# Optimization experiments

Measured on AMD Instinct MI355X. Metric: run time of the kernel, lower is better.

Reference implementation:

```python
import jax, jax.numpy as jnp
import numpy as np

B, N, DIM = 2, 2048, 1024
HEADS, DIM_HEAD, ROT = 16, 64, 32
SCALE = DIM_HEAD ** -0.5
INNER = HEADS * DIM_HEAD


def rotate_half(x):
    # '... (j d) -> ... j d' with j=2 -> split into first/second half
    d = x.shape[-1] // 2
    x1, x2 = x[..., :d], x[..., d:]
    return jnp.concatenate([-x2, x1], axis=-1)


def apply_rotary_pos_emb(freqs, t):
    rot = freqs.shape[-1]
    t1, t_pass = t[..., :rot], t[..., rot:]
    t1 = t1 * jnp.cos(freqs) + rotate_half(t1) * jnp.sin(freqs)
    return jnp.concatenate([t1, t_pass], axis=-1)


def setup_inputs() -> dict:
    key = jax.random.key(0)
    ks = jax.random.split(key, 5)
    x = jax.random.normal(ks[0], (B, N, DIM), dtype=jnp.float32)
    mask = jnp.ones((B, N), dtype=bool)
    rotary_pos_emb = jax.random.normal(ks[1], (N, ROT), dtype=jnp.float32)
    w_qkv = jax.random.normal(ks[2], (DIM, 3 * INNER), dtype=jnp.float32) * (DIM ** -0.5)
    w_out = jax.random.normal(ks[3], (INNER, DIM), dtype=jnp.float32) * (INNER ** -0.5)
    g = jnp.ones((DIM,), dtype=jnp.float32)
    return {"x": x, "mask": mask, "rotary_pos_emb": rotary_pos_emb,
            "w_qkv": w_qkv, "w_out": w_out, "g": g}


def reference(x, mask, rotary_pos_emb, w_qkv, w_out, g):
    b, n, _ = x.shape
    qkv = x @ w_qkv  # [b, n, 3*inner]
    q, k, v = jnp.split(qkv, 3, axis=-1)
    def to_heads(t):
        return t.reshape(b, n, HEADS, DIM_HEAD).transpose(0, 2, 1, 3)  # b h n d
    q, k, v = to_heads(q), to_heads(k), to_heads(v)
    q = q * SCALE
    # note: original applies rotary to q, k AND v
    q = apply_rotary_pos_emb(rotary_pos_emb, q)
    k = apply_rotary_pos_emb(rotary_pos_emb, k)
    v = apply_rotary_pos_emb(rotary_pos_emb, v)
    sim = jnp.einsum('bhid,bhjd->bhij', q, k)  # [b, h, n, n]
    neg = -jnp.finfo(sim.dtype).max
    sim = jnp.where(mask[:, None, None, :], sim, neg)
    causal_mask = jnp.triu(jnp.ones((n, n), dtype=bool), 1)
    sim = jnp.where(causal_mask, neg, sim)
    attn = jax.nn.softmax(sim.astype(jnp.float32), axis=-1).astype(sim.dtype)
    out = jnp.einsum('bhij,bhjd->bhid', attn, v)
    out = out.transpose(0, 2, 1, 3).reshape(b, n, INNER)
    out = out @ w_out
    # LayerNorm (no bias), eps=1e-5 for fp32, biased variance
    mean = jnp.mean(out, axis=-1, keepdims=True)
    var = jnp.var(out, axis=-1, keepdims=True)
    return (out - mean) * jax.lax.rsqrt(var + 1e-5) * g
```

## Files before the change

kernel.cpp:

```cpp
#include <hip/hip_runtime.h>
#include <stdint.h>

typedef unsigned short u16;
typedef __bf16 bf16x8 __attribute__((ext_vector_type(8)));
typedef float f32x4 __attribute__((ext_vector_type(4)));

#define B_ 2
#define N_ 2048
#define H_ 16
#define SCALE_ 0.125f
#define FM_ 11.0f

__device__ __forceinline__ float b2f(u16 u) {
    unsigned v = (unsigned)u << 16;
    float f;
    __builtin_memcpy(&f, &v, 4);
    return f;
}
__device__ __forceinline__ u16 f2b(float f) {
    unsigned x;
    __builtin_memcpy(&x, &f, 4);
    x = x + 0x7fff + ((x >> 16) & 1);
    return (u16)(x >> 16);
}
__device__ __forceinline__ unsigned fbits(float f) {
    unsigned x;
    __builtin_memcpy(&x, &f, 4);
    return x;
}

typedef const __attribute__((address_space(1))) unsigned int ga_uint;
typedef __attribute__((address_space(3))) unsigned int ls_uint;
__device__ __forceinline__ void gld_lds16(const void* g, void* l) {
    __builtin_amdgcn_global_load_lds((ga_uint*)g, (ls_uint*)l, 16, 0, 0);
}

#define MFMA_ __builtin_amdgcn_mfma_f32_16x16x32_bf16
#define ZERO4_ ((f32x4){0.f, 0.f, 0.f, 0.f})

__global__ __launch_bounds__(256) void sentinel(float* __restrict__ out, int n, float val) {
    int i = blockIdx.x * 256 + threadIdx.x;
    if (i < n) out[i] = val;
}

__global__ __launch_bounds__(256) void prep(const float* __restrict__ rotf,
                                            float* __restrict__ ct, float* __restrict__ st,
                                            const float* __restrict__ x, u16* __restrict__ xbf,
                                            const float* __restrict__ wqkv, u16* __restrict__ wqkvT,
                                            const float* __restrict__ wout, u16* __restrict__ woutT) {
    __shared__ float tile[32][33];
    int bid = blockIdx.x;
    const int tid = threadIdx.x;
    if (bid < 256) {
        int i = bid * 256 + tid;
        float f = rotf[i];
        ct[i] = cosf(f);
        st[i] = sinf(f);
        return;
    }
    bid -= 256;
    if (bid < 4096) {
        int i = (bid * 256 + tid) * 4;
        float4 v = *(const float4*)(x + i);
        ushort4 o;
        o.x = f2b(v.x); o.y = f2b(v.y); o.z = f2b(v.z); o.w = f2b(v.w);
        *(ushort4*)(xbf + i) = o;
        return;
    }
    bid -= 4096;
    const float* in;
    u16* out;
    int C, bx, by;
    if (bid < 3072) {
        in = wqkv; out = wqkvT; C = 3072; bx = bid % 96; by = bid / 96;
    } else {
        bid -= 3072;
        in = wout; out = woutT; C = 1024; bx = bid % 32; by = bid / 32;
    }
    const int R = 1024;
    int tx = tid & 31, ty = tid >> 5;
    int c0 = bx * 32, r0 = by * 32;
#pragma unroll
    for (int i = 0; i < 32; i += 8) tile[ty + i][tx] = in[(size_t)(r0 + ty + i) * C + c0 + tx];
    __syncthreads();
#pragma unroll
    for (int i = 0; i < 32; i += 8) out[(size_t)(c0 + ty + i) * R + r0 + tx] = f2b(tile[tx][ty + i]);
}

__global__ __launch_bounds__(256) void gemm_qkv(const u16* __restrict__ A, const u16* __restrict__ Bt,
                                                const float* __restrict__ ct, const float* __restrict__ st,
                                                u16* __restrict__ qo, u16* __restrict__ ko,
                                                u16* __restrict__ vt) {
    __shared__ __align__(16) u16 As[2][128 * 32];
    __shared__ __align__(16) u16 Bs[2][128 * 32];
    const int tid = threadIdx.x;
    const int wave = tid >> 6, lane = tid & 63;
    const int l15 = lane & 15, q4 = lane >> 4;
    const int id = blockIdx.x;
    const int xcd = id & 7, slot = id >> 3;
    const int nt = (xcd & 1) * 12 + (slot % 12);
    const int mt = (xcd >> 1) * 8 + (slot / 12);
    const int m0 = mt * 128, n0 = nt * 128;
    const int wm = (wave & 1) * 64, wn = (wave >> 1) * 64;
    const int lrow = lane >> 2, lchunk = (lane & 3) * 8;

    auto stage = [&](int buf, int k0) {
        int r0_ = wave * 32, r1_ = r0_ + 16;
        gld_lds16(&A[(size_t)(m0 + r0_ + lrow) * 1024 + k0 + lchunk], &As[buf][r0_ * 32]);
        gld_lds16(&Bt[(size_t)(n0 + r0_ + lrow) * 1024 + k0 + lchunk], &Bs[buf][r0_ * 32]);
        gld_lds16(&A[(size_t)(m0 + r1_ + lrow) * 1024 + k0 + lchunk], &As[buf][r1_ * 32]);
        gld_lds16(&Bt[(size_t)(n0 + r1_ + lrow) * 1024 + k0 + lchunk], &Bs[buf][r1_ * 32]);
    };

    f32x4 c00 = ZERO4_, c01 = ZERO4_, c02 = ZERO4_, c03 = ZERO4_;
    f32x4 c10 = ZERO4_, c11 = ZERO4_, c12 = ZERO4_, c13 = ZERO4_;
    f32x4 c20 = ZERO4_, c21 = ZERO4_, c22 = ZERO4_, c23 = ZERO4_;
    f32x4 c30 = ZERO4_, c31 = ZERO4_, c32 = ZERO4_, c33 = ZERO4_;

    stage(0, 0);
    __syncthreads();
    for (int t = 0; t < 32; ++t) {
        const int cur = t & 1;
        if (t < 31) stage(cur ^ 1, (t + 1) * 32);
        bf16x8 a0 = *(const bf16x8*)&As[cur][(wm + l15) * 32 + q4 * 8];
        bf16x8 a1 = *(const bf16x8*)&As[cur][(wm + 16 + l15) * 32 + q4 * 8];
        bf16x8 a2 = *(const bf16x8*)&As[cur][(wm + 32 + l15) * 32 + q4 * 8];
        bf16x8 a3 = *(const bf16x8*)&As[cur][(wm + 48 + l15) * 32 + q4 * 8];
        bf16x8 b0 = *(const bf16x8*)&Bs[cur][(wn + l15) * 32 + q4 * 8];
        bf16x8 b1 = *(const bf16x8*)&Bs[cur][(wn + 16 + l15) * 32 + q4 * 8];
        bf16x8 b2 = *(const bf16x8*)&Bs[cur][(wn + 32 + l15) * 32 + q4 * 8];
        bf16x8 b3 = *(const bf16x8*)&Bs[cur][(wn + 48 + l15) * 32 + q4 * 8];
        c00 = MFMA_(a0, b0, c00, 0, 0, 0); c01 = MFMA_(a0, b1, c01, 0, 0, 0);
        c02 = MFMA_(a0, b2, c02, 0, 0, 0); c03 = MFMA_(a0, b3, c03, 0, 0, 0);
        c10 = MFMA_(a1, b0, c10, 0, 0, 0); c11 = MFMA_(a1, b1, c11, 0, 0, 0);
        c12 = MFMA_(a1, b2, c12, 0, 0, 0); c13 = MFMA_(a1, b3, c13, 0, 0, 0);
        c20 = MFMA_(a2, b0, c20, 0, 0, 0); c21 = MFMA_(a2, b1, c21, 0, 0, 0);
        c22 = MFMA_(a2, b2, c22, 0, 0, 0); c23 = MFMA_(a2, b3, c23, 0, 0, 0);
        c30 = MFMA_(a3, b0, c30, 0, 0, 0); c31 = MFMA_(a3, b1, c31, 0, 0, 0);
        c32 = MFMA_(a3, b2, c32, 0, 0, 0); c33 = MFMA_(a3, b3, c33, 0, 0, 0);
        if (t < 31) __syncthreads();
    }
    const int qh = n0 + wn;
    const int t = qh >> 10;
    const int h = (qh & 1023) >> 6;
    auto epi = [&](int mtb, f32x4 x0v, f32x4 x1v, f32x4 x2v, f32x4 x3v) {
#pragma unroll
        for (int r = 0; r < 4; r++) {
            int gm = m0 + wm + mtb + q4 * 4 + r;
            int b = gm >> 11, n = gm & 2047;
            float x0 = x0v[r], x1 = x1v[r], x2 = x2v[r], x3 = x3v[r];
            float c1 = ct[n * 32 + l15], s1 = st[n * 32 + l15];
            float c2 = ct[n * 32 + 16 + l15], s2 = st[n * 32 + 16 + l15];
            if (t == 0) { x0 *= SCALE_; x1 *= SCALE_; x2 *= SCALE_; x3 *= SCALE_; }
            float r0 = x0 * c1 - x1 * s1;
            float r1 = x1 * c2 + x0 * s2;
            int bh = b * H_ + h;
            if (t == 2) {
                u16* o = vt + (size_t)bh * 64 * N_;
                o[(l15) * N_ + n] = f2b(r0);
                o[(l15 + 16) * N_ + n] = f2b(r1);
                o[(l15 + 32) * N_ + n] = f2b(x2);
                o[(l15 + 48) * N_ + n] = f2b(x3);
            } else {
                u16* dst = (t == 0) ? qo : ko;
                u16* p = dst + ((size_t)bh * N_ + n) * 64;
                p[l15] = f2b(r0);
                p[l15 + 16] = f2b(r1);
                p[l15 + 32] = f2b(x2);
                p[l15 + 48] = f2b(x3);
            }
        }
    };
    epi(0, c00, c01, c02, c03);
    epi(16, c10, c11, c12, c13);
    epi(32, c20, c21, c22, c23);
    epi(48, c30, c31, c32, c33);
}

__global__ __launch_bounds__(256) void attn(const u16* __restrict__ q, const u16* __restrict__ k,
                                            const u16* __restrict__ vt, u16* __restrict__ out) {
    __shared__ __align__(16) u16 Ks[2][64 * 72];
    __shared__ __align__(16) u16 Vs[2][64 * 72];
    __shared__ __align__(16) u16 Ps[64 * 72];
    const int tid = threadIdx.x, wave = tid >> 6, lane = tid & 63;
    const int l15 = lane & 15, q4 = lane >> 4;
    const int id = blockIdx.x;
    const int slot = id >> 3;
    const int bh = (id & 7) * 4 + (slot >> 4);
    const int ta = slot & 15, tb = 31 - ta;
    const u16* qp = q + (size_t)bh * N_ * 64;
    const u16* kp = k + (size_t)bh * N_ * 64;
    const u16* vp = vt + (size_t)bh * 64 * N_;
    const int b = bh >> 4, h = bh & 15;
    const int srow8 = tid >> 3, scol8 = (tid & 7) * 8;
    const int prow = (wave * 16 + l15) * 72;

    bf16x8 aqA0, aqA1, aqB0, aqB1;
    {
        int qr = ta * 64 + wave * 16;
        aqA0 = *(const bf16x8*)&qp[(qr + l15) * 64 + q4 * 8];
        aqA1 = *(const bf16x8*)&qp[(qr + l15) * 64 + 32 + q4 * 8];
        qr = tb * 64 + wave * 16;
        aqB0 = *(const bf16x8*)&qp[(qr + l15) * 64 + q4 * 8];
        aqB1 = *(const bf16x8*)&qp[(qr + l15) * 64 + 32 + q4 * 8];
    }
    f32x4 o[4];
#pragma unroll
    for (int i = 0; i < 4; i++) o[i] = ZERO4_;
    float psum = 0.f;

    uint4 LK0, LK1, LV0, LV1;
    auto ldissue = [&](int jt) {
        LK0 = *(const uint4*)&kp[(size_t)(jt * 64 + srow8) * 64 + scol8];
        LK1 = *(const uint4*)&kp[(size_t)(jt * 64 + 32 + srow8) * 64 + scol8];
        LV0 = *(const uint4*)&vp[(size_t)srow8 * N_ + jt * 64 + scol8];
        LV1 = *(const uint4*)&vp[(size_t)(32 + srow8) * N_ + jt * 64 + scol8];
    };
    auto wrbuf = [&](int buf) {
        *(uint4*)&Ks[buf][srow8 * 72 + scol8] = LK0;
        *(uint4*)&Ks[buf][(32 + srow8) * 72 + scol8] = LK1;
        *(uint4*)&Vs[buf][srow8 * 72 + scol8] = LV0;
        *(uint4*)&Vs[buf][(32 + srow8) * 72 + scol8] = LV1;
    };
    auto tileof = [&](int i) { return (i <= ta) ? i : i - ta - 1; };

    auto iter = [&](bf16x8 aq0, bf16x8 aq1, int cur, int domask, int qa, int jb) {
#pragma unroll
        for (int kt = 0; kt < 4; kt++) {
            bf16x8 kf0 = *(const bf16x8*)&Ks[cur][(kt * 16 + l15) * 72 + q4 * 8];
            bf16x8 kf1 = *(const bf16x8*)&Ks[cur][(kt * 16 + l15) * 72 + 32 + q4 * 8];
            f32x4 z = ZERO4_;
            z = MFMA_(kf0, aq0, z, 0, 0, 0);
            z = MFMA_(kf1, aq1, z, 0, 0, 0);
            float p0, p1, p2, p3;
            {
                float s0 = z[0], s1 = z[1], s2 = z[2], s3 = z[3];
                if (domask) {
                    int key = jb * 64 + kt * 16 + q4 * 4;
                    if (key + 0 > qa) s0 = -1e30f;
                    if (key + 1 > qa) s1 = -1e30f;
                    if (key + 2 > qa) s2 = -1e30f;
                    if (key + 3 > qa) s3 = -1e30f;
                }
                p0 = __expf(s0 - FM_); p1 = __expf(s1 - FM_);
                p2 = __expf(s2 - FM_); p3 = __expf(s3 - FM_);
            }
            psum += (p0 + p1) + (p2 + p3);
            uint2 pk;
            pk.x = __builtin_amdgcn_perm(fbits(p1), fbits(p0), 0x07060302u);
            pk.y = __builtin_amdgcn_perm(fbits(p3), fbits(p2), 0x07060302u);
            *(uint2*)&Ps[prow + kt * 16 + q4 * 4] = pk;
        }
        bf16x8 pf0 = *(const bf16x8*)&Ps[prow + q4 * 8];
        bf16x8 pf1 = *(const bf16x8*)&Ps[prow + 32 + q4 * 8];
#pragma unroll
        for (int dt = 0; dt < 4; dt++) {
            bf16x8 v0 = *(const bf16x8*)&Vs[cur][(dt * 16 + l15) * 72 + q4 * 8];
            bf16x8 v1 = *(const bf16x8*)&Vs[cur][(dt * 16 + l15) * 72 + 32 + q4 * 8];
            o[dt] = MFMA_(v0, pf0, o[dt], 0, 0, 0);
            o[dt] = MFMA_(v1, pf1, o[dt], 0, 0, 0);
        }
    };
    auto epilogue = [&](int qt) {
        float v = psum;
        v += __shfl_xor(v, 16);
        v += __shfl_xor(v, 32);
        float inv = 1.f / v;
        int n = qt * 64 + wave * 16 + l15;
        u16* op = out + ((size_t)b * N_ + n) * 1024 + h * 64;
#pragma unroll
        for (int dt = 0; dt < 4; dt++) {
            union { u16 u[4]; uint2 v2; } w;
#pragma unroll
            for (int r = 0; r < 4; r++) w.u[r] = f2b(o[dt][r] * inv);
            *(uint2*)(op + dt * 16 + q4 * 4) = w.v2;
        }
#pragma unroll
        for (int i = 0; i < 4; i++) o[i] = ZERO4_;
        psum = 0.f;
    };

    ldissue(0);
    wrbuf(0);
    ldissue(tileof(1));
    int m = 0;
    for (int jb = 0; jb <= ta; jb++, m++) {
        const int cur = m & 1;
        asm volatile("s_waitcnt lgkmcnt(0)" ::: "memory");
        __builtin_amdgcn_s_barrier();
        iter(aqA0, aqA1, cur, jb == ta, ta * 64 + wave * 16 + l15, jb);
        wrbuf(cur ^ 1);
        ldissue(tileof(m + 2));
    }
    epilogue(ta);
    for (int jb = 0; jb <= tb; jb++, m++) {
        const int cur = m & 1;
        asm volatile("s_waitcnt lgkmcnt(0)" ::: "memory");
        __builtin_amdgcn_s_barrier();
        iter(aqB0, aqB1, cur, jb == tb, tb * 64 + wave * 16 + l15, jb);
        if (m < 32) {
            wrbuf(cur ^ 1);
            if (m < 31) ldissue(tileof(m + 2));
        }
    }
    epilogue(tb);
}

__global__ __launch_bounds__(256) void gemm_out(const u16* __restrict__ A, const u16* __restrict__ Bt,
                                                float* __restrict__ C) {
    __shared__ __align__(16) u16 As[2][128 * 32];
    __shared__ __align__(16) u16 Bs[2][128 * 32];
    const int tid = threadIdx.x;
    const int wave = tid >> 6, lane = tid & 63;
    const int l15 = lane & 15, q4 = lane >> 4;
    const int id = blockIdx.x;
    const int xcd = id & 7, slot = id >> 3;
    const int mt = xcd * 4 + (slot >> 3);
    const int nt = slot & 7;
    const int m0 = mt * 128, n0 = nt * 128;
    const int wm = (wave & 1) * 64, wn = (wave >> 1) * 64;
    const int lrow = lane >> 2, lchunk = (lane & 3) * 8;

    auto stage = [&](int buf, int k0) {
        int r0_ = wave * 32, r1_ = r0_ + 16;
        gld_lds16(&A[(size_t)(m0 + r0_ + lrow) * 1024 + k0 + lchunk], &As[buf][r0_ * 32]);
        gld_lds16(&Bt[(size_t)(n0 + r0_ + lrow) * 1024 + k0 + lchunk], &Bs[buf][r0_ * 32]);
        gld_lds16(&A[(size_t)(m0 + r1_ + lrow) * 1024 + k0 + lchunk], &As[buf][r1_ * 32]);
        gld_lds16(&Bt[(size_t)(n0 + r1_ + lrow) * 1024 + k0 + lchunk], &Bs[buf][r1_ * 32]);
    };

    f32x4 c00 = ZERO4_, c01 = ZERO4_, c02 = ZERO4_, c03 = ZERO4_;
    f32x4 c10 = ZERO4_, c11 = ZERO4_, c12 = ZERO4_, c13 = ZERO4_;
    f32x4 c20 = ZERO4_, c21 = ZERO4_, c22 = ZERO4_, c23 = ZERO4_;
    f32x4 c30 = ZERO4_, c31 = ZERO4_, c32 = ZERO4_, c33 = ZERO4_;

    stage(0, 0);
    __syncthreads();
    for (int t = 0; t < 32; ++t) {
        const int cur = t & 1;
        if (t < 31) stage(cur ^ 1, (t + 1) * 32);
        bf16x8 a0 = *(const bf16x8*)&As[cur][(wm + l15) * 32 + q4 * 8];
        bf16x8 a1 = *(const bf16x8*)&As[cur][(wm + 16 + l15) * 32 + q4 * 8];
        bf16x8 a2 = *(const bf16x8*)&As[cur][(wm + 32 + l15) * 32 + q4 * 8];
        bf16x8 a3 = *(const bf16x8*)&As[cur][(wm + 48 + l15) * 32 + q4 * 8];
        bf16x8 b0 = *(const bf16x8*)&Bs[cur][(wn + l15) * 32 + q4 * 8];
        bf16x8 b1 = *(const bf16x8*)&Bs[cur][(wn + 16 + l15) * 32 + q4 * 8];
        bf16x8 b2 = *(const bf16x8*)&Bs[cur][(wn + 32 + l15) * 32 + q4 * 8];
        bf16x8 b3 = *(const bf16x8*)&Bs[cur][(wn + 48 + l15) * 32 + q4 * 8];
        c00 = MFMA_(a0, b0, c00, 0, 0, 0); c01 = MFMA_(a0, b1, c01, 0, 0, 0);
        c02 = MFMA_(a0, b2, c02, 0, 0, 0); c03 = MFMA_(a0, b3, c03, 0, 0, 0);
        c10 = MFMA_(a1, b0, c10, 0, 0, 0); c11 = MFMA_(a1, b1, c11, 0, 0, 0);
        c12 = MFMA_(a1, b2, c12, 0, 0, 0); c13 = MFMA_(a1, b3, c13, 0, 0, 0);
        c20 = MFMA_(a2, b0, c20, 0, 0, 0); c21 = MFMA_(a2, b1, c21, 0, 0, 0);
        c22 = MFMA_(a2, b2, c22, 0, 0, 0); c23 = MFMA_(a2, b3, c23, 0, 0, 0);
        c30 = MFMA_(a3, b0, c30, 0, 0, 0); c31 = MFMA_(a3, b1, c31, 0, 0, 0);
        c32 = MFMA_(a3, b2, c32, 0, 0, 0); c33 = MFMA_(a3, b3, c33, 0, 0, 0);
        if (t < 31) __syncthreads();
    }
    auto sto = [&](int mtb, int ntb, f32x4 c) {
#pragma unroll
        for (int r = 0; r < 4; r++) {
            int gm = m0 + wm + mtb + q4 * 4 + r;
            int gn = n0 + wn + ntb + l15;
            C[(size_t)gm * 1024 + gn] = c[r];
        }
    };
    sto(0, 0, c00);  sto(0, 16, c01);  sto(0, 32, c02);  sto(0, 48, c03);
    sto(16, 0, c10); sto(16, 16, c11); sto(16, 32, c12); sto(16, 48, c13);
    sto(32, 0, c20); sto(32, 16, c21); sto(32, 32, c22); sto(32, 48, c23);
    sto(48, 0, c30); sto(48, 16, c31); sto(48, 32, c32); sto(48, 48, c33);
}

__global__ __launch_bounds__(256) void lnorm(const float* __restrict__ x, const float* __restrict__ g,
                                             float* __restrict__ out) {
    __shared__ float sh[8];
    int row = blockIdx.x, tid = threadIdx.x;
    float4 v = *(const float4*)(x + (size_t)row * 1024 + tid * 4);
    float s = v.x + v.y + v.z + v.w;
    float sq = v.x * v.x + v.y * v.y + v.z * v.z + v.w * v.w;
#pragma unroll
    for (int m = 1; m < 64; m <<= 1) {
        s += __shfl_xor(s, m);
        sq += __shfl_xor(sq, m);
    }
    if ((tid & 63) == 0) {
        sh[tid >> 6] = s;
        sh[4 + (tid >> 6)] = sq;
    }
    __syncthreads();
    s = sh[0] + sh[1] + sh[2] + sh[3];
    sq = sh[4] + sh[5] + sh[6] + sh[7];
    float mean = s * (1.f / 1024.f);
    float var = fmaxf(sq * (1.f / 1024.f) - mean * mean, 0.f);
    float rstd = rsqrtf(var + 1e-5f);
    float4 gv = *(const float4*)(g + tid * 4);
    float4 ov;
    ov.x = (v.x - mean) * rstd * gv.x;
    ov.y = (v.y - mean) * rstd * gv.y;
    ov.z = (v.z - mean) * rstd * gv.z;
    ov.w = (v.w - mean) * rstd * gv.w;
    *(float4*)(out + (size_t)row * 1024 + tid * 4) = ov;
}

extern "C" void kernel_launch(void* const* d_in, const int* in_sizes, int n_in,
                              void* d_out, int out_size, void* d_ws, size_t ws_size,
                              hipStream_t stream) {
    const float* x = nullptr;
    const float* rotf = nullptr;
    const float* wqkv = nullptr;
    const float* wout = nullptr;
    const float* g = nullptr;
    for (int i = 0; i < n_in; i++) {
        switch (in_sizes[i]) {
            case 4194304: x = (const float*)d_in[i]; break;
            case 65536:   rotf = (const float*)d_in[i]; break;
            case 3145728: wqkv = (const float*)d_in[i]; break;
            case 1048576: wout = (const float*)d_in[i]; break;
            case 1024:    g = (const float*)d_in[i]; break;
            default: break;
        }
    }
    int oblk = (out_size + 255) / 256;
    if (!(x && rotf && wqkv && wout && g)) {
        sentinel<<<oblk, 256, 0, stream>>>((float*)d_out, out_size, 200.f);
        return;
    }
    const size_t MB = 1024u * 1024;
    if (ws_size < 80 * MB) {
        sentinel<<<oblk, 256, 0, stream>>>((float*)d_out, out_size, 100.f);
        return;
    }
    char* ws = (char*)d_ws;
    u16* wqkvT = (u16*)(ws);
    u16* woutT = (u16*)(ws + 6 * MB);
    u16* xbf = (u16*)(ws + 8 * MB);
    u16* qbuf = (u16*)(ws + 16 * MB);
    u16* kbuf = (u16*)(ws + 24 * MB);
    u16* vtbuf = (u16*)(ws + 32 * MB);
    u16* abuf = (u16*)(ws + 40 * MB);
    float* pbuf = (float*)(ws + 48 * MB);
    float* ctab = (float*)(ws + 64 * MB);
    float* stab = (float*)(ws + 64 * MB + 256 * 1024);

    prep<<<8448, 256, 0, stream>>>(rotf, ctab, stab, x, xbf, wqkv, wqkvT, wout, woutT);
    gemm_qkv<<<768, 256, 0, stream>>>(xbf, wqkvT, ctab, stab, qbuf, kbuf, vtbuf);
    attn<<<512, 256, 0, stream>>>(qbuf, kbuf, vtbuf, abuf);
    gemm_out<<<256, 256, 0, stream>>>(abuf, woutT, pbuf);
    lnorm<<<4096, 256, 0, stream>>>(pbuf, g, (float*)d_out);
}
```

Measured before the change: 201.3 us.

## Swizzle GEMM LDS tiles and drop double buffering in qkv/out GEMMs

Both projection GEMMs now write global-to-LDS loads into an XOR-swizzled layout. The loading lanes' global addresses are remapped by an inverse swizzle, and the MFMA operand reads use swizzled offsets, to avoid LDS bank conflicts on the 16-byte fragment reads. The double-buffered prefetch is replaced by a single buffer with load, sync, compute, sync each K step. This halves LDS use and may raise occupancy, but global-load latency is no longer overlapped with MFMA work within a block.

```diff
diff --git a/kernel.cpp b/kernel.cpp
--- a/kernel.cpp
+++ b/kernel.cpp
@@ -87,12 +87,21 @@
     for (int i = 0; i < 32; i += 8) out[(size_t)(c0 + ty + i) * R + r0 + tx] = f2b(tile[tx][ty + i]);
 }
 
+__device__ __forceinline__ int swz_off(int row, int c16) {
+    return (((row * 64 + c16 * 16) ^ ((row & 7) << 4)) >> 1);
+}
+__device__ __forceinline__ void swz_inv(int W, int& r, int& c16) {
+    int rh = W >> 7;
+    r = (rh << 1) | (((W >> 6) & 1) ^ ((rh >> 1) & 1));
+    c16 = ((W >> 4) & 3) ^ (r & 3);
+}
+
 __global__ __launch_bounds__(256) void gemm_qkv(const u16* __restrict__ A, const u16* __restrict__ Bt,
                                                 const float* __restrict__ ct, const float* __restrict__ st,
                                                 u16* __restrict__ qo, u16* __restrict__ ko,
                                                 u16* __restrict__ vt) {
-    __shared__ __align__(16) u16 As[2][128 * 32];
-    __shared__ __align__(16) u16 Bs[2][128 * 32];
+    __shared__ __align__(16) u16 As[128 * 32];
+    __shared__ __align__(16) u16 Bs[128 * 32];
     const int tid = threadIdx.x;
     const int wave = tid >> 6, lane = tid & 63;
     const int l15 = lane & 15, q4 = lane >> 4;
@@ -102,34 +111,39 @@
     const int mt = (xcd >> 1) * 8 + (slot / 12);
     const int m0 = mt * 128, n0 = nt * 128;
     const int wm = (wave & 1) * 64, wn = (wave >> 1) * 64;
-    const int lrow = lane >> 2, lchunk = (lane & 3) * 8;
-
-    auto stage = [&](int buf, int k0) {
-        int r0_ = wave * 32, r1_ = r0_ + 16;
-        gld_lds16(&A[(size_t)(m0 + r0_ + lrow) * 1024 + k0 + lchunk], &As[buf][r0_ * 32]);
-        gld_lds16(&Bt[(size_t)(n0 + r0_ + lrow) * 1024 + k0 + lchunk], &Bs[buf][r0_ * 32]);
-        gld_lds16(&A[(size_t)(m0 + r1_ + lrow) * 1024 + k0 + lchunk], &As[buf][r1_ * 32]);
-        gld_lds16(&Bt[(size_t)(n0 + r1_ + lrow) * 1024 + k0 + lchunk], &Bs[buf][r1_ * 32]);
-    };
+
+    int rS0, cS0, rS1, cS1;
+    swz_inv((wave * 32) * 64 + lane * 16, rS0, cS0);
+    swz_inv((wave * 32 + 16) * 64 + lane * 16, rS1, cS1);
+    const u16* aS0 = A + (size_t)(m0 + rS0) * 1024 + cS0 * 8;
+    const u16* aS1 = A + (size_t)(m0 + rS1) * 1024 + cS1 * 8;
+    const u16* bS0 = Bt + (size_t)(n0 + rS0) * 1024 + cS0 * 8;
+    const u16* bS1 = Bt + (size_t)(n0 + rS1) * 1024 + cS1 * 8;
+
+    const int oa0 = swz_off(wm + l15, q4), oa1 = swz_off(wm + 16 + l15, q4),
+              oa2 = swz_off(wm + 32 + l15, q4), oa3 = swz_off(wm + 48 + l15, q4);
+    const int ob0 = swz_off(wn + l15, q4), ob1 = swz_off(wn + 16 + l15, q4),
+              ob2 = swz_off(wn + 32 + l15, q4), ob3 = swz_off(wn + 48 + l15, q4);
 
     f32x4 c00 = ZERO4_, c01 = ZERO4_, c02 = ZERO4_, c03 = ZERO4_;
     f32x4 c10 = ZERO4_, c11 = ZERO4_, c12 = ZERO4_, c13 = ZERO4_;
     f32x4 c20 = ZERO4_, c21 = ZERO4_, c22 = ZERO4_, c23 = ZERO4_;
     f32x4 c30 = ZERO4_, c31 = ZERO4_, c32 = ZERO4_, c33 = ZERO4_;
 
-    stage(0, 0);
-    __syncthreads();
-    for (int t = 0; t < 32; ++t) {
-        const int cur = t & 1;
-        if (t < 31) stage(cur ^ 1, (t + 1) * 32);
-        bf16x8 a0 = *(const bf16x8*)&As[cur][(wm + l15) * 32 + q4 * 8];
-        bf16x8 a1 = *(const bf16x8*)&As[cur][(wm + 16 + l15) * 32 + q4 * 8];
-        bf16x8 a2 = *(const bf16x8*)&As[cur][(wm + 32 + l15) * 32 + q4 * 8];
-        bf16x8 a3 = *(const bf16x8*)&As[cur][(wm + 48 + l15) * 32 + q4 * 8];
-        bf16x8 b0 = *(const bf16x8*)&Bs[cur][(wn + l15) * 32 + q4 * 8];
-        bf16x8 b1 = *(const bf16x8*)&Bs[cur][(wn + 16 + l15) * 32 + q4 * 8];
-        bf16x8 b2 = *(const bf16x8*)&Bs[cur][(wn + 32 + l15) * 32 + q4 * 8];
-        bf16x8 b3 = *(const bf16x8*)&Bs[cur][(wn + 48 + l15) * 32 + q4 * 8];
+    for (int k0 = 0; k0 < 1024; k0 += 32) {
+        gld_lds16(aS0 + k0, &As[(wave * 32) * 32]);
+        gld_lds16(bS0 + k0, &Bs[(wave * 32) * 32]);
+        gld_lds16(aS1 + k0, &As[(wave * 32 + 16) * 32]);
+        gld_lds16(bS1 + k0, &Bs[(wave * 32 + 16) * 32]);
+        __syncthreads();
+        bf16x8 a0 = *(const bf16x8*)&As[oa0];
+        bf16x8 a1 = *(const bf16x8*)&As[oa1];
+        bf16x8 a2 = *(const bf16x8*)&As[oa2];
+        bf16x8 a3 = *(const bf16x8*)&As[oa3];
+        bf16x8 b0 = *(const bf16x8*)&Bs[ob0];
+        bf16x8 b1 = *(const bf16x8*)&Bs[ob1];
+        bf16x8 b2 = *(const bf16x8*)&Bs[ob2];
+        bf16x8 b3 = *(const bf16x8*)&Bs[ob3];
         c00 = MFMA_(a0, b0, c00, 0, 0, 0); c01 = MFMA_(a0, b1, c01, 0, 0, 0);
         c02 = MFMA_(a0, b2, c02, 0, 0, 0); c03 = MFMA_(a0, b3, c03, 0, 0, 0);
         c10 = MFMA_(a1, b0, c10, 0, 0, 0); c11 = MFMA_(a1, b1, c11, 0, 0, 0);
@@ -138,7 +152,7 @@
         c22 = MFMA_(a2, b2, c22, 0, 0, 0); c23 = MFMA_(a2, b3, c23, 0, 0, 0);
         c30 = MFMA_(a3, b0, c30, 0, 0, 0); c31 = MFMA_(a3, b1, c31, 0, 0, 0);
         c32 = MFMA_(a3, b2, c32, 0, 0, 0); c33 = MFMA_(a3, b3, c33, 0, 0, 0);
-        if (t < 31) __syncthreads();
+        __syncthreads();
     }
     const int qh = n0 + wn;
     const int t = qh >> 10;
@@ -308,8 +322,8 @@
 
 __global__ __launch_bounds__(256) void gemm_out(const u16* __restrict__ A, const u16* __restrict__ Bt,
                                                 float* __restrict__ C) {
-    __shared__ __align__(16) u16 As[2][128 * 32];
-    __shared__ __align__(16) u16 Bs[2][128 * 32];
+    __shared__ __align__(16) u16 As[128 * 32];
+    __shared__ __align__(16) u16 Bs[128 * 32];
     const int tid = threadIdx.x;
     const int wave = tid >> 6, lane = tid & 63;
     const int l15 = lane & 15, q4 = lane >> 4;
@@ -319,34 +333,39 @@
     const int nt = slot & 7;
     const int m0 = mt * 128, n0 = nt * 128;
     const int wm = (wave & 1) * 64, wn = (wave >> 1) * 64;
-    const int lrow = lane >> 2, lchunk = (lane & 3) * 8;
-
-    auto stage = [&](int buf, int k0) {
-        int r0_ = wave * 32, r1_ = r0_ + 16;
-        gld_lds16(&A[(size_t)(m0 + r0_ + lrow) * 1024 + k0 + lchunk], &As[buf][r0_ * 32]);
-        gld_lds16(&Bt[(size_t)(n0 + r0_ + lrow) * 1024 + k0 + lchunk], &Bs[buf][r0_ * 32]);
-        gld_lds16(&A[(size_t)(m0 + r1_ + lrow) * 1024 + k0 + lchunk], &As[buf][r1_ * 32]);
-        gld_lds16(&Bt[(size_t)(n0 + r1_ + lrow) * 1024 + k0 + lchunk], &Bs[buf][r1_ * 32]);
-    };
+
+    int rS0, cS0, rS1, cS1;
+    swz_inv((wave * 32) * 64 + lane * 16, rS0, cS0);
+    swz_inv((wave * 32 + 16) * 64 + lane * 16, rS1, cS1);
+    const u16* aS0 = A + (size_t)(m0 + rS0) * 1024 + cS0 * 8;
+    const u16* aS1 = A + (size_t)(m0 + rS1) * 1024 + cS1 * 8;
+    const u16* bS0 = Bt + (size_t)(n0 + rS0) * 1024 + cS0 * 8;
+    const u16* bS1 = Bt + (size_t)(n0 + rS1) * 1024 + cS1 * 8;
+
+    const int oa0 = swz_off(wm + l15, q4), oa1 = swz_off(wm + 16 + l15, q4),
+              oa2 = swz_off(wm + 32 + l15, q4), oa3 = swz_off(wm + 48 + l15, q4);
+    const int ob0 = swz_off(wn + l15, q4), ob1 = swz_off(wn + 16 + l15, q4),
+              ob2 = swz_off(wn + 32 + l15, q4), ob3 = swz_off(wn + 48 + l15, q4);
 
     f32x4 c00 = ZERO4_, c01 = ZERO4_, c02 = ZERO4_, c03 = ZERO4_;
     f32x4 c10 = ZERO4_, c11 = ZERO4_, c12 = ZERO4_, c13 = ZERO4_;
     f32x4 c20 = ZERO4_, c21 = ZERO4_, c22 = ZERO4_, c23 = ZERO4_;
     f32x4 c30 = ZERO4_, c31 = ZERO4_, c32 = ZERO4_, c33 = ZERO4_;
 
-    stage(0, 0);
-    __syncthreads();
-    for (int t = 0; t < 32; ++t) {
-        const int cur = t & 1;
-        if (t < 31) stage(cur ^ 1, (t + 1) * 32);
-        bf16x8 a0 = *(const bf16x8*)&As[cur][(wm + l15) * 32 + q4 * 8];
-        bf16x8 a1 = *(const bf16x8*)&As[cur][(wm + 16 + l15) * 32 + q4 * 8];
-        bf16x8 a2 = *(const bf16x8*)&As[cur][(wm + 32 + l15) * 32 + q4 * 8];
-        bf16x8 a3 = *(const bf16x8*)&As[cur][(wm + 48 + l15) * 32 + q4 * 8];
-        bf16x8 b0 = *(const bf16x8*)&Bs[cur][(wn + l15) * 32 + q4 * 8];
-        bf16x8 b1 = *(const bf16x8*)&Bs[cur][(wn + 16 + l15) * 32 + q4 * 8];
-        bf16x8 b2 = *(const bf16x8*)&Bs[cur][(wn + 32 + l15) * 32 + q4 * 8];
-        bf16x8 b3 = *(const bf16x8*)&Bs[cur][(wn + 48 + l15) * 32 + q4 * 8];
+    for (int k0 = 0; k0 < 1024; k0 += 32) {
+        gld_lds16(aS0 + k0, &As[(wave * 32) * 32]);
+        gld_lds16(bS0 + k0, &Bs[(wave * 32) * 32]);
+        gld_lds16(aS1 + k0, &As[(wave * 32 + 16) * 32]);
+        gld_lds16(bS1 + k0, &Bs[(wave * 32 + 16) * 32]);
+        __syncthreads();
+        bf16x8 a0 = *(const bf16x8*)&As[oa0];
+        bf16x8 a1 = *(const bf16x8*)&As[oa1];
+        bf16x8 a2 = *(const bf16x8*)&As[oa2];
+        bf16x8 a3 = *(const bf16x8*)&As[oa3];
+        bf16x8 b0 = *(const bf16x8*)&Bs[ob0];
+        bf16x8 b1 = *(const bf16x8*)&Bs[ob1];
+        bf16x8 b2 = *(const bf16x8*)&Bs[ob2];
+        bf16x8 b3 = *(const bf16x8*)&Bs[ob3];
         c00 = MFMA_(a0, b0, c00, 0, 0, 0); c01 = MFMA_(a0, b1, c01, 0, 0, 0);
         c02 = MFMA_(a0, b2, c02, 0, 0, 0); c03 = MFMA_(a0, b3, c03, 0, 0, 0);
         c10 = MFMA_(a1, b0, c10, 0, 0, 0); c11 = MFMA_(a1, b1, c11, 0, 0, 0);
@@ -355,7 +374,7 @@
         c22 = MFMA_(a2, b2, c22, 0, 0, 0); c23 = MFMA_(a2, b3, c23, 0, 0, 0);
         c30 = MFMA_(a3, b0, c30, 0, 0, 0); c31 = MFMA_(a3, b1, c31, 0, 0, 0);
         c32 = MFMA_(a3, b2, c32, 0, 0, 0); c33 = MFMA_(a3, b3, c33, 0, 0, 0);
-        if (t < 31) __syncthreads();
+        __syncthreads();
     }
     auto sto = [&](int mtb, int ntb, f32x4 c) {
 #pragma unroll
```

After: 202.0 us. Within noise of the previous version (+0.3%).

## Use single-buffered K=64 XOR-swizzled LDS tiles in QKV and output GEMMs

Applied to the files above, without the earlier changes.

Both projection GEMMs now load 64-wide K slices per step into a single LDS buffer instead of double-buffering 32-wide slices. An XOR swizzle on the 16-byte chunk index is applied during the global-to-LDS copy and again in the fragment reads, aiming to avoid LDS bank conflicts. This halves the number of barrier iterations but gives up the overlap between the next tile's global loads and the current tile's MFMAs, so load latency becomes exposed each iteration.

```diff
diff --git a/kernel.cpp b/kernel.cpp
--- a/kernel.cpp
+++ b/kernel.cpp
@@ -87,12 +87,13 @@
     for (int i = 0; i < 32; i += 8) out[(size_t)(c0 + ty + i) * R + r0 + tx] = f2b(tile[tx][ty + i]);
 }
 
+
 __global__ __launch_bounds__(256) void gemm_qkv(const u16* __restrict__ A, const u16* __restrict__ Bt,
                                                 const float* __restrict__ ct, const float* __restrict__ st,
                                                 u16* __restrict__ qo, u16* __restrict__ ko,
                                                 u16* __restrict__ vt) {
-    __shared__ __align__(16) u16 As[2][128 * 32];
-    __shared__ __align__(16) u16 Bs[2][128 * 32];
+    __shared__ __align__(16) u16 As[128 * 64];
+    __shared__ __align__(16) u16 Bs[128 * 64];
     const int tid = threadIdx.x;
     const int wave = tid >> 6, lane = tid & 63;
     const int l15 = lane & 15, q4 = lane >> 4;
@@ -102,43 +103,51 @@
     const int mt = (xcd >> 1) * 8 + (slot / 12);
     const int m0 = mt * 128, n0 = nt * 128;
     const int wm = (wave & 1) * 64, wn = (wave >> 1) * 64;
-    const int lrow = lane >> 2, lchunk = (lane & 3) * 8;
-
-    auto stage = [&](int buf, int k0) {
-        int r0_ = wave * 32, r1_ = r0_ + 16;
-        gld_lds16(&A[(size_t)(m0 + r0_ + lrow) * 1024 + k0 + lchunk], &As[buf][r0_ * 32]);
-        gld_lds16(&Bt[(size_t)(n0 + r0_ + lrow) * 1024 + k0 + lchunk], &Bs[buf][r0_ * 32]);
-        gld_lds16(&A[(size_t)(m0 + r1_ + lrow) * 1024 + k0 + lchunk], &As[buf][r1_ * 32]);
-        gld_lds16(&Bt[(size_t)(n0 + r1_ + lrow) * 1024 + k0 + lchunk], &Bs[buf][r1_ * 32]);
-    };
+
+    const int srow = lane >> 3;
+    const int sc16 = (lane & 7) ^ srow;
+    const u16* aSrc = A + (size_t)(m0 + wave * 32 + srow) * 1024 + sc16 * 8;
+    const u16* bSrc = Bt + (size_t)(n0 + wave * 32 + srow) * 1024 + sc16 * 8;
+
+    const int pa0 = (wm + l15) * 64, pa1 = (wm + 16 + l15) * 64,
+              pa2 = (wm + 32 + l15) * 64, pa3 = (wm + 48 + l15) * 64;
+    const int pb0 = (wn + l15) * 64, pb1 = (wn + 16 + l15) * 64,
+              pb2 = (wn + 32 + l15) * 64, pb3 = (wn + 48 + l15) * 64;
+    const int x7 = l15 & 7;
 
     f32x4 c00 = ZERO4_, c01 = ZERO4_, c02 = ZERO4_, c03 = ZERO4_;
     f32x4 c10 = ZERO4_, c11 = ZERO4_, c12 = ZERO4_, c13 = ZERO4_;
     f32x4 c20 = ZERO4_, c21 = ZERO4_, c22 = ZERO4_, c23 = ZERO4_;
     f32x4 c30 = ZERO4_, c31 = ZERO4_, c32 = ZERO4_, c33 = ZERO4_;
 
-    stage(0, 0);
-    __syncthreads();
-    for (int t = 0; t < 32; ++t) {
-        const int cur = t & 1;
-        if (t < 31) stage(cur ^ 1, (t + 1) * 32);
-        bf16x8 a0 = *(const bf16x8*)&As[cur][(wm + l15) * 32 + q4 * 8];
-        bf16x8 a1 = *(const bf16x8*)&As[cur][(wm + 16 + l15) * 32 + q4 * 8];
-        bf16x8 a2 = *(const bf16x8*)&As[cur][(wm + 32 + l15) * 32 + q4 * 8];
-        bf16x8 a3 = *(const bf16x8*)&As[cur][(wm + 48 + l15) * 32 + q4 * 8];
-        bf16x8 b0 = *(const bf16x8*)&Bs[cur][(wn + l15) * 32 + q4 * 8];
-        bf16x8 b1 = *(const bf16x8*)&Bs[cur][(wn + 16 + l15) * 32 + q4 * 8];
-        bf16x8 b2 = *(const bf16x8*)&Bs[cur][(wn + 32 + l15) * 32 + q4 * 8];
-        bf16x8 b3 = *(const bf16x8*)&Bs[cur][(wn + 48 + l15) * 32 + q4 * 8];
-        c00 = MFMA_(a0, b0, c00, 0, 0, 0); c01 = MFMA_(a0, b1, c01, 0, 0, 0);
-        c02 = MFMA_(a0, b2, c02, 0, 0, 0); c03 = MFMA_(a0, b3, c03, 0, 0, 0);
-        c10 = MFMA_(a1, b0, c10, 0, 0, 0); c11 = MFMA_(a1, b1, c11, 0, 0, 0);
-        c12 = MFMA_(a1, b2, c12, 0, 0, 0); c13 = MFMA_(a1, b3, c13, 0, 0, 0);
-        c20 = MFMA_(a2, b0, c20, 0, 0, 0); c21 = MFMA_(a2, b1, c21, 0, 0, 0);
-        c22 = MFMA_(a2, b2, c22, 0, 0, 0); c23 = MFMA_(a2, b3, c23, 0, 0, 0);
-        c30 = MFMA_(a3, b0, c30, 0, 0, 0); c31 = MFMA_(a3, b1, c31, 0, 0, 0);
-        c32 = MFMA_(a3, b2, c32, 0, 0, 0); c33 = MFMA_(a3, b3, c33, 0, 0, 0);
-        if (t < 31) __syncthreads();
+    for (int k0 = 0; k0 < 1024; k0 += 64) {
+#pragma unroll
+        for (int i = 0; i < 4; i++) {
+            gld_lds16(aSrc + (size_t)(i * 8) * 1024 + k0, &As[wave * 2048 + i * 512]);
+            gld_lds16(bSrc + (size_t)(i * 8) * 1024 + k0, &Bs[wave * 2048 + i * 512]);
+        }
+        __syncthreads();
+#pragma unroll
+        for (int kk = 0; kk < 2; kk++) {
+            const int co = ((kk * 4 + q4) ^ x7) * 8;
+            bf16x8 a0 = *(const bf16x8*)&As[pa0 + co];
+            bf16x8 a1 = *(const bf16x8*)&As[pa1 + co];
+            bf16x8 a2 = *(const bf16x8*)&As[pa2 + co];
+            bf16x8 a3 = *(const bf16x8*)&As[pa3 + co];
+            bf16x8 b0 = *(const bf16x8*)&Bs[pb0 + co];
+            bf16x8 b1 = *(const bf16x8*)&Bs[pb1 + co];
+            bf16x8 b2 = *(const bf16x8*)&Bs[pb2 + co];
+            bf16x8 b3 = *(const bf16x8*)&Bs[pb3 + co];
+            c00 = MFMA_(a0, b0, c00, 0, 0, 0); c01 = MFMA_(a0, b1, c01, 0, 0, 0);
+            c02 = MFMA_(a0, b2, c02, 0, 0, 0); c03 = MFMA_(a0, b3, c03, 0, 0, 0);
+            c10 = MFMA_(a1, b0, c10, 0, 0, 0); c11 = MFMA_(a1, b1, c11, 0, 0, 0);
+            c12 = MFMA_(a1, b2, c12, 0, 0, 0); c13 = MFMA_(a1, b3, c13, 0, 0, 0);
+            c20 = MFMA_(a2, b0, c20, 0, 0, 0); c21 = MFMA_(a2, b1, c21, 0, 0, 0);
+            c22 = MFMA_(a2, b2, c22, 0, 0, 0); c23 = MFMA_(a2, b3, c23, 0, 0, 0);
+            c30 = MFMA_(a3, b0, c30, 0, 0, 0); c31 = MFMA_(a3, b1, c31, 0, 0, 0);
+            c32 = MFMA_(a3, b2, c32, 0, 0, 0); c33 = MFMA_(a3, b3, c33, 0, 0, 0);
+        }
+        __syncthreads();
     }
     const int qh = n0 + wn;
     const int t = qh >> 10;
@@ -308,8 +317,8 @@
 
 __global__ __launch_bounds__(256) void gemm_out(const u16* __restrict__ A, const u16* __restrict__ Bt,
                                                 float* __restrict__ C) {
-    __shared__ __align__(16) u16 As[2][128 * 32];
-    __shared__ __align__(16) u16 Bs[2][128 * 32];
+    __shared__ __align__(16) u16 As[128 * 64];
+    __shared__ __align__(16) u16 Bs[128 * 64];
     const int tid = threadIdx.x;
     const int wave = tid >> 6, lane = tid & 63;
     const int l15 = lane & 15, q4 = lane >> 4;
@@ -319,43 +328,51 @@
     const int nt = slot & 7;
     const int m0 = mt * 128, n0 = nt * 128;
     const int wm = (wave & 1) * 64, wn = (wave >> 1) * 64;
-    const int lrow = lane >> 2, lchunk = (lane & 3) * 8;
-
-    auto stage = [&](int buf, int k0) {
-        int r0_ = wave * 32, r1_ = r0_ + 16;
-        gld_lds16(&A[(size_t)(m0 + r0_ + lrow) * 1024 + k0 + lchunk], &As[buf][r0_ * 32]);
-        gld_lds16(&Bt[(size_t)(n0 + r0_ + lrow) * 1024 + k0 + lchunk], &Bs[buf][r0_ * 32]);
-        gld_lds16(&A[(size_t)(m0 + r1_ + lrow) * 1024 + k0 + lchunk], &As[buf][r1_ * 32]);
-        gld_lds16(&Bt[(size_t)(n0 + r1_ + lrow) * 1024 + k0 + lchunk], &Bs[buf][r1_ * 32]);
-    };
+
+    const int srow = lane >> 3;
+    const int sc16 = (lane & 7) ^ srow;
+    const u16* aSrc = A + (size_t)(m0 + wave * 32 + srow) * 1024 + sc16 * 8;
+    const u16* bSrc = Bt + (size_t)(n0 + wave * 32 + srow) * 1024 + sc16 * 8;
+
+    const int pa0 = (wm + l15) * 64, pa1 = (wm + 16 + l15) * 64,
+              pa2 = (wm + 32 + l15) * 64, pa3 = (wm + 48 + l15) * 64;
+    const int pb0 = (wn + l15) * 64, pb1 = (wn + 16 + l15) * 64,
+              pb2 = (wn + 32 + l15) * 64, pb3 = (wn + 48 + l15) * 64;
+    const int x7 = l15 & 7;
 
     f32x4 c00 = ZERO4_, c01 = ZERO4_, c02 = ZERO4_, c03 = ZERO4_;
     f32x4 c10 = ZERO4_, c11 = ZERO4_, c12 = ZERO4_, c13 = ZERO4_;
     f32x4 c20 = ZERO4_, c21 = ZERO4_, c22 = ZERO4_, c23 = ZERO4_;
     f32x4 c30 = ZERO4_, c31 = ZERO4_, c32 = ZERO4_, c33 = ZERO4_;
 
-    stage(0, 0);
-    __syncthreads();
-    for (int t = 0; t < 32; ++t) {
-        const int cur = t & 1;
-        if (t < 31) stage(cur ^ 1, (t + 1) * 32);
-        bf16x8 a0 = *(const bf16x8*)&As[cur][(wm + l15) * 32 + q4 * 8];
-        bf16x8 a1 = *(const bf16x8*)&As[cur][(wm + 16 + l15) * 32 + q4 * 8];
-        bf16x8 a2 = *(const bf16x8*)&As[cur][(wm + 32 + l15) * 32 + q4 * 8];
-        bf16x8 a3 = *(const bf16x8*)&As[cur][(wm + 48 + l15) * 32 + q4 * 8];
-        bf16x8 b0 = *(const bf16x8*)&Bs[cur][(wn + l15) * 32 + q4 * 8];
-        bf16x8 b1 = *(const bf16x8*)&Bs[cur][(wn + 16 + l15) * 32 + q4 * 8];
-        bf16x8 b2 = *(const bf16x8*)&Bs[cur][(wn + 32 + l15) * 32 + q4 * 8];
-        bf16x8 b3 = *(const bf16x8*)&Bs[cur][(wn + 48 + l15) * 32 + q4 * 8];
-        c00 = MFMA_(a0, b0, c00, 0, 0, 0); c01 = MFMA_(a0, b1, c01, 0, 0, 0);
-        c02 = MFMA_(a0, b2, c02, 0, 0, 0); c03 = MFMA_(a0, b3, c03, 0, 0, 0);
-        c10 = MFMA_(a1, b0, c10, 0, 0, 0); c11 = MFMA_(a1, b1, c11, 0, 0, 0);
-        c12 = MFMA_(a1, b2, c12, 0, 0, 0); c13 = MFMA_(a1, b3, c13, 0, 0, 0);
-        c20 = MFMA_(a2, b0, c20, 0, 0, 0); c21 = MFMA_(a2, b1, c21, 0, 0, 0);
-        c22 = MFMA_(a2, b2, c22, 0, 0, 0); c23 = MFMA_(a2, b3, c23, 0, 0, 0);
-        c30 = MFMA_(a3, b0, c30, 0, 0, 0); c31 = MFMA_(a3, b1, c31, 0, 0, 0);
-        c32 = MFMA_(a3, b2, c32, 0, 0, 0); c33 = MFMA_(a3, b3, c33, 0, 0, 0);
-        if (t < 31) __syncthreads();
+    for (int k0 = 0; k0 < 1024; k0 += 64) {
+#pragma unroll
+        for (int i = 0; i < 4; i++) {
+            gld_lds16(aSrc + (size_t)(i * 8) * 1024 + k0, &As[wave * 2048 + i * 512]);
+            gld_lds16(bSrc + (size_t)(i * 8) * 1024 + k0, &Bs[wave * 2048 + i * 512]);
+        }
+        __syncthreads();
+#pragma unroll
+        for (int kk = 0; kk < 2; kk++) {
+            const int co = ((kk * 4 + q4) ^ x7) * 8;
+            bf16x8 a0 = *(const bf16x8*)&As[pa0 + co];
+            bf16x8 a1 = *(const bf16x8*)&As[pa1 + co];
+            bf16x8 a2 = *(const bf16x8*)&As[pa2 + co];
+            bf16x8 a3 = *(const bf16x8*)&As[pa3 + co];
+            bf16x8 b0 = *(const bf16x8*)&Bs[pb0 + co];
+            bf16x8 b1 = *(const bf16x8*)&Bs[pb1 + co];
+            bf16x8 b2 = *(const bf16x8*)&Bs[pb2 + co];
+            bf16x8 b3 = *(const bf16x8*)&Bs[pb3 + co];
+            c00 = MFMA_(a0, b0, c00, 0, 0, 0); c01 = MFMA_(a0, b1, c01, 0, 0, 0);
+            c02 = MFMA_(a0, b2, c02, 0, 0, 0); c03 = MFMA_(a0, b3, c03, 0, 0, 0);
+            c10 = MFMA_(a1, b0, c10, 0, 0, 0); c11 = MFMA_(a1, b1, c11, 0, 0, 0);
+            c12 = MFMA_(a1, b2, c12, 0, 0, 0); c13 = MFMA_(a1, b3, c13, 0, 0, 0);
+            c20 = MFMA_(a2, b0, c20, 0, 0, 0); c21 = MFMA_(a2, b1, c21, 0, 0, 0);
+            c22 = MFMA_(a2, b2, c22, 0, 0, 0); c23 = MFMA_(a2, b3, c23, 0, 0, 0);
+            c30 = MFMA_(a3, b0, c30, 0, 0, 0); c31 = MFMA_(a3, b1, c31, 0, 0, 0);
+            c32 = MFMA_(a3, b2, c32, 0, 0, 0); c33 = MFMA_(a3, b3, c33, 0, 0, 0);
+        }
+        __syncthreads();
     }
     auto sto = [&](int mtb, int ntb, f32x4 c) {
 #pragma unroll
```

Measured after the change: 209.9 us. +4.3%, slower.
